# Optimization experiments

Hardware: AMD Instinct MI355X
Metric: run time of the kernel (lower is better)

Reference implementation:

```python
import jax, jax.numpy as jnp
import numpy as np

N_NODES = 500000
N_GRAPHS = 4096
D_LOCAL = 64
D_GLOBAL = 64
D_HIDDEN = 128
D_PRE = 64
LN_EPS = 1e-5


def _layer_norm(x, g, b):
    mu = jnp.mean(x, axis=-1, keepdims=True)
    var = jnp.var(x, axis=-1, keepdims=True)
    return (x - mu) * jax.lax.rsqrt(var + LN_EPS) * g + b


def setup_inputs() -> dict:
    key = jax.random.key(0)
    ks = jax.random.split(key, 16)
    s = 0.02
    d_concat = D_LOCAL + D_GLOBAL  # 128
    d_post_in = D_PRE + D_GLOBAL   # 128
    return {
        "x": jax.random.normal(ks[0], (N_NODES, D_LOCAL), jnp.float32),
        "u": jax.random.normal(ks[1], (N_GRAPHS, D_GLOBAL), jnp.float32),
        "batch": jax.random.randint(ks[2], (N_NODES,), 0, N_GRAPHS, jnp.int64),
        # mlp_pre_aggr params
        "w1": jax.random.normal(ks[3], (d_concat, D_HIDDEN), jnp.float32) * s,
        "b1": jnp.zeros((D_HIDDEN,), jnp.float32),
        "w2": jax.random.normal(ks[4], (D_HIDDEN, D_HIDDEN), jnp.float32) * s,
        "b2": jnp.zeros((D_HIDDEN,), jnp.float32),
        "w3": jax.random.normal(ks[5], (D_HIDDEN, D_PRE), jnp.float32) * s,
        "b3": jnp.zeros((D_PRE,), jnp.float32),
        "ln1_g": jnp.ones((D_PRE,), jnp.float32),
        "ln1_b": jnp.zeros((D_PRE,), jnp.float32),
        # mlp_post_aggr params
        "w4": jax.random.normal(ks[6], (d_post_in, D_HIDDEN), jnp.float32) * s,
        "b4": jnp.zeros((D_HIDDEN,), jnp.float32),
        "w5": jax.random.normal(ks[7], (D_HIDDEN, D_HIDDEN), jnp.float32) * s,
        "b5": jnp.zeros((D_HIDDEN,), jnp.float32),
        "w6": jax.random.normal(ks[8], (D_HIDDEN, D_GLOBAL), jnp.float32) * s,
        "b6": jnp.zeros((D_GLOBAL,), jnp.float32),
        "ln2_g": jnp.ones((D_GLOBAL,), jnp.float32),
        "ln2_b": jnp.zeros((D_GLOBAL,), jnp.float32),
    }


def reference(x, u, batch, w1, b1, w2, b2, w3, b3, ln1_g, ln1_b,
              w4, b4, w5, b5, w6, b6, ln2_g, ln2_b):
    # gather global state to nodes and concat: [N, dim_local + dim_global]
    h = jnp.concatenate([x, u[batch]], axis=-1)
    # mlp_pre_aggr (dropout p=0 -> identity)
    h = jax.nn.relu(h @ w1 + b1)
    h = jax.nn.relu(h @ w2 + b2)
    h = _layer_norm(h @ w3 + b3, ln1_g, ln1_b)  # [N, dim_pre_aggr]
    # scatter_add per graph
    agg = jax.ops.segment_sum(h, batch, num_segments=u.shape[0])  # [B, dim_pre_aggr]
    # concat with u, mlp_post_aggr
    g = jnp.concatenate([agg, u], axis=-1)
    g = jax.nn.relu(g @ w4 + b4)
    g = jax.nn.relu(g @ w5 + b5)
    g = _layer_norm(g @ w6 + b6, ln2_g, ln2_b)
    return g + u
```

## Files before the change

### kernel.cpp

```cpp
#include <hip/hip_runtime.h>
#include <hip/hip_bf16.h>
#include <stdint.h>


#define NNODES 500000
#define NGRAPHS 4096
#define ROWS 128
#define LDH 136

typedef __attribute__((ext_vector_type(8))) _Float16 half8;
typedef __attribute__((ext_vector_type(4))) float floatx4;

__global__ void prep_kernel(const float* __restrict__ w1, const float* __restrict__ w2,
                            const float* __restrict__ w3,
                            _Float16* __restrict__ w1T, _Float16* __restrict__ w2T,
                            _Float16* __restrict__ w3T) {
    int i = blockIdx.x * 256 + threadIdx.x;
    if (i < 128 * 128) {
        int n = i >> 7, k = i & 127;
        w1T[i] = (_Float16)w1[k * 128 + n];
        w2T[i] = (_Float16)w2[k * 128 + n];
    }
    if (i < 64 * 128) {
        int n = i >> 7, k = i & 127;
        w3T[i] = (_Float16)w3[k * 64 + n];
    }
}

__global__ __launch_bounds__(256, 2) void node_kernel(
    const float* __restrict__ x, const float* __restrict__ u, const int* __restrict__ batch,
    const _Float16* __restrict__ w1T, const _Float16* __restrict__ w2T,
    const _Float16* __restrict__ w3T,
    const float* __restrict__ b1, const float* __restrict__ b2, const float* __restrict__ b3,
    const float* __restrict__ lng, const float* __restrict__ lnb,
    float* __restrict__ agg)
{
    __shared__ __align__(16) _Float16 hA[ROWS * LDH];
    __shared__ int sBatch[ROWS];

    const int tid = threadIdx.x;
    const int rowbase = blockIdx.x * ROWS;
    const int wave = tid >> 6;
    const int lane = tid & 63;
    const int q = lane >> 4;
    const int l16 = lane & 15;

    for (int r = tid; r < ROWS; r += 256) {
        int gr = rowbase + r;
        sBatch[r] = (gr < NNODES) ? batch[gr] : 0;
    }
    __syncthreads();

    for (int i = tid; i < ROWS * 16; i += 256) {
        int r = i >> 4, c4 = (i & 15) << 2;
        int gr = rowbase + r;
        float4 vx = make_float4(0.f, 0.f, 0.f, 0.f);
        if (gr < NNODES) vx = *(const float4*)(x + (size_t)gr * 64 + c4);
        _Float16* p = &hA[r * LDH + c4];
        p[0] = (_Float16)vx.x; p[1] = (_Float16)vx.y;
        p[2] = (_Float16)vx.z; p[3] = (_Float16)vx.w;
        int g = sBatch[r];
        float4 vu = *(const float4*)(u + (size_t)g * 64 + c4);
        _Float16* p2 = &hA[r * LDH + 64 + c4];
        p2[0] = (_Float16)vu.x; p2[1] = (_Float16)vu.y;
        p2[2] = (_Float16)vu.z; p2[3] = (_Float16)vu.w;
    }
    __syncthreads();

    const int rowg = (wave >> 1) * 64;
    const int colg = (wave & 1) * 64;
    for (int layer = 0; layer < 2; ++layer) {
        const _Float16* wT = layer ? w2T : w1T;
        const float* bias = layer ? b2 : b1;
        floatx4 acc[4][4];
        #pragma unroll
        for (int ct = 0; ct < 4; ++ct) {
            float bv = bias[colg + ct * 16 + l16];
            #pragma unroll
            for (int rt = 0; rt < 4; ++rt) acc[rt][ct] = (floatx4){bv, bv, bv, bv};
        }
        half8 bfr[4][4];
        #pragma unroll
        for (int ks = 0; ks < 4; ++ks)
            #pragma unroll
            for (int ct = 0; ct < 4; ++ct)
                bfr[ks][ct] = *(const half8*)(wT + (colg + ct * 16 + l16) * 128 + ks * 32 + q * 8);
        #pragma unroll
        for (int ks = 0; ks < 4; ++ks) {
            half8 af[4];
            #pragma unroll
            for (int rt = 0; rt < 4; ++rt)
                af[rt] = *(const half8*)(&hA[(rowg + rt * 16 + l16) * LDH + ks * 32 + q * 8]);
            #pragma unroll
            for (int rt = 0; rt < 4; ++rt)
                #pragma unroll
                for (int ct = 0; ct < 4; ++ct)
                    acc[rt][ct] = __builtin_amdgcn_mfma_f32_16x16x32_f16(
                        af[rt], bfr[ks][ct], acc[rt][ct], 0, 0, 0);
        }
        __syncthreads();
        #pragma unroll
        for (int rt = 0; rt < 4; ++rt)
            #pragma unroll
            for (int ct = 0; ct < 4; ++ct)
                #pragma unroll
                for (int j = 0; j < 4; ++j) {
                    float v = acc[rt][ct][j];
                    v = v > 0.f ? v : 0.f;
                    hA[(rowg + rt * 16 + q * 4 + j) * LDH + colg + ct * 16 + l16] = (_Float16)v;
                }
        __syncthreads();
    }

    {
        const int rowg3 = wave * 32;
        floatx4 acc[2][4];
        #pragma unroll
        for (int ct = 0; ct < 4; ++ct) {
            float bv = b3[ct * 16 + l16];
            acc[0][ct] = (floatx4){bv, bv, bv, bv};
            acc[1][ct] = (floatx4){bv, bv, bv, bv};
        }
        half8 bfr[4][4];
        #pragma unroll
        for (int ks = 0; ks < 4; ++ks)
            #pragma unroll
            for (int ct = 0; ct < 4; ++ct)
                bfr[ks][ct] = *(const half8*)(w3T + (ct * 16 + l16) * 128 + ks * 32 + q * 8);
        #pragma unroll
        for (int ks = 0; ks < 4; ++ks) {
            half8 af[2];
            #pragma unroll
            for (int rt = 0; rt < 2; ++rt)
                af[rt] = *(const half8*)(&hA[(rowg3 + rt * 16 + l16) * LDH + ks * 32 + q * 8]);
            #pragma unroll
            for (int rt = 0; rt < 2; ++rt)
                #pragma unroll
                for (int ct = 0; ct < 4; ++ct)
                    acc[rt][ct] = __builtin_amdgcn_mfma_f32_16x16x32_f16(
                        af[rt], bfr[ks][ct], acc[rt][ct], 0, 0, 0);
        }
        float gct[4], bct[4];
        #pragma unroll
        for (int ct = 0; ct < 4; ++ct) {
            gct[ct] = lng[ct * 16 + l16];
            bct[ct] = lnb[ct * 16 + l16];
        }
        #pragma unroll
        for (int rt = 0; rt < 2; ++rt)
            #pragma unroll
            for (int j = 0; j < 4; ++j) {
                int rloc = rowg3 + rt * 16 + q * 4 + j;
                float v0 = acc[rt][0][j], v1 = acc[rt][1][j];
                float v2 = acc[rt][2][j], v3 = acc[rt][3][j];
                float s = v0 + v1 + v2 + v3;
                float ss = v0 * v0 + v1 * v1 + v2 * v2 + v3 * v3;
                #pragma unroll
                for (int m = 1; m < 16; m <<= 1) {
                    s += __shfl_xor(s, m, 16);
                    ss += __shfl_xor(ss, m, 16);
                }
                float mean = s * (1.f / 64.f);
                float var = ss * (1.f / 64.f) - mean * mean;
                float rstd = rsqrtf(var + 1e-5f);
                if (rowbase + rloc < NNODES) {
                    float* dst = agg + (size_t)sBatch[rloc] * 64;
                    unsafeAtomicAdd(dst + 0 + l16,  (v0 - mean) * rstd * gct[0] + bct[0]);
                    unsafeAtomicAdd(dst + 16 + l16, (v1 - mean) * rstd * gct[1] + bct[1]);
                    unsafeAtomicAdd(dst + 32 + l16, (v2 - mean) * rstd * gct[2] + bct[2]);
                    unsafeAtomicAdd(dst + 48 + l16, (v3 - mean) * rstd * gct[3] + bct[3]);
                }
            }
    }
}

__global__ __launch_bounds__(256, 4) void graph_kernel(
    const float* __restrict__ u,
    const float* __restrict__ w4, const float* __restrict__ b4,
    const float* __restrict__ w5, const float* __restrict__ b5,
    const float* __restrict__ w6, const float* __restrict__ b6,
    const float* __restrict__ g2, const float* __restrict__ bb2,
    float* __restrict__ out)
{
    __shared__ float z[4][2][128];
    const int wave = threadIdx.x >> 6, lane = threadIdx.x & 63;
    const int g = blockIdx.x * 4 + wave;
    float* za = z[wave][0];
    float* zb = z[wave][1];
    za[lane] = out[(size_t)g * 64 + lane];
    za[64 + lane] = u[(size_t)g * 64 + lane];
    float s0 = b4[lane], s1 = b4[64 + lane];
    for (int k = 0; k < 128; ++k) {
        float zk = za[k];
        s0 = fmaf(zk, w4[k * 128 + lane], s0);
        s1 = fmaf(zk, w4[k * 128 + 64 + lane], s1);
    }
    zb[lane] = fmaxf(s0, 0.f); zb[64 + lane] = fmaxf(s1, 0.f);
    s0 = b5[lane]; s1 = b5[64 + lane];
    for (int k = 0; k < 128; ++k) {
        float zk = zb[k];
        s0 = fmaf(zk, w5[k * 128 + lane], s0);
        s1 = fmaf(zk, w5[k * 128 + 64 + lane], s1);
    }
    za[lane] = fmaxf(s0, 0.f); za[64 + lane] = fmaxf(s1, 0.f);
    float s = b6[lane];
    for (int k = 0; k < 128; ++k) s = fmaf(za[k], w6[k * 64 + lane], s);
    float sum = s, ssq = s * s;
    #pragma unroll
    for (int m = 1; m < 64; m <<= 1) {
        sum += __shfl_xor(sum, m, 64);
        ssq += __shfl_xor(ssq, m, 64);
    }
    float mean = sum * (1.f / 64.f);
    float var = ssq * (1.f / 64.f) - mean * mean;
    float rstd = rsqrtf(var + 1e-5f);
    out[(size_t)g * 64 + lane] =
        (s - mean) * rstd * g2[lane] + bb2[lane] + u[(size_t)g * 64 + lane];
}

extern "C" void kernel_launch(void* const* d_in, const int* in_sizes, int n_in,
                              void* d_out, int out_size, void* d_ws, size_t ws_size,
                              hipStream_t stream) {
    const float* x   = (const float*)d_in[0];
    const float* u   = (const float*)d_in[1];
    const int*   bt  = (const int*)d_in[2];
    const float* w1  = (const float*)d_in[3];
    const float* b1  = (const float*)d_in[4];
    const float* w2  = (const float*)d_in[5];
    const float* b2  = (const float*)d_in[6];
    const float* w3  = (const float*)d_in[7];
    const float* b3  = (const float*)d_in[8];
    const float* lng = (const float*)d_in[9];
    const float* lnb = (const float*)d_in[10];
    const float* w4  = (const float*)d_in[11];
    const float* b4  = (const float*)d_in[12];
    const float* w5  = (const float*)d_in[13];
    const float* b5  = (const float*)d_in[14];
    const float* w6  = (const float*)d_in[15];
    const float* b6  = (const float*)d_in[16];
    const float* g2  = (const float*)d_in[17];
    const float* bb2 = (const float*)d_in[18];
    float* out = (float*)d_out;

    _Float16* w1T = (_Float16*)d_ws;
    _Float16* w2T = w1T + 128 * 128;
    _Float16* w3T = w2T + 128 * 128;

    hipMemsetAsync(d_out, 0, (size_t)NGRAPHS * 64 * sizeof(float), stream);
    prep_kernel<<<64, 256, 0, stream>>>(w1, w2, w3, w1T, w2T, w3T);
    node_kernel<<<(NNODES + ROWS - 1) / ROWS, 256, 0, stream>>>(
        x, u, bt, w1T, w2T, w3T, b1, b2, b3, lng, lnb, out);
    graph_kernel<<<NGRAPHS / 4, 256, 0, stream>>>(
        u, w4, b4, w5, b5, w6, b6, g2, bb2, out);
}
```

Before: 408.4 us.

## Sort nodes by graph and fuse per-graph node MLP, aggregation and post-MLP

Builds a counting sort of nodes by graph id (histogram, scan, scatter) and launches one block per graph. Each block gathers its nodes' x rows, runs the three-layer node MLP and layer norm, sums the results in registers and runs the post-aggregation MLP directly. This removes the float atomics into agg and the separate graph kernel. The u part of the first layer is computed once per graph as a bias, halving that layer's K dimension. The cost is three extra small kernels, gathered x loads, and uneven per-graph work with only 4096 blocks and partially filled last tiles.

Result: slower. 707.7 us (+73.3%).

```diff
diff --git a/kernel.cpp b/kernel.cpp
--- a/kernel.cpp
+++ b/kernel.cpp
@@ -5,7 +5,6 @@
 
 #define NNODES 500000
 #define NGRAPHS 4096
-#define ROWS 128
 #define LDH 136
 
 typedef __attribute__((ext_vector_type(8))) _Float16 half8;
@@ -27,195 +26,303 @@
     }
 }
 
-__global__ __launch_bounds__(256, 2) void node_kernel(
-    const float* __restrict__ x, const float* __restrict__ u, const int* __restrict__ batch,
+__global__ void hist_kernel(const int* __restrict__ batch, int* __restrict__ cnt) {
+    int i = blockIdx.x * 256 + threadIdx.x;
+    if (i < NNODES) atomicAdd(&cnt[batch[i]], 1);
+}
+
+__global__ void scan_kernel(const int* __restrict__ cnt, int* __restrict__ offs) {
+    __shared__ int ssum[256];
+    int t = threadIdx.x;
+    int base = t * 16;
+    int s = 0;
+    #pragma unroll
+    for (int j = 0; j < 16; ++j) s += cnt[base + j];
+    ssum[t] = s;
+    __syncthreads();
+    for (int d = 1; d < 256; d <<= 1) {
+        int v = (t >= d) ? ssum[t - d] : 0;
+        __syncthreads();
+        ssum[t] += v;
+        __syncthreads();
+    }
+    int run = ssum[t] - s;
+    #pragma unroll
+    for (int j = 0; j < 16; ++j) { offs[base + j] = run; run += cnt[base + j]; }
+    if (t == 255) offs[4096] = run;
+}
+
+__global__ void scatter_kernel(const int* __restrict__ batch, const int* __restrict__ offs,
+                               int* __restrict__ cursor, int* __restrict__ sorted) {
+    int i = blockIdx.x * 256 + threadIdx.x;
+    if (i < NNODES) {
+        int g = batch[i];
+        int p = offs[g] + atomicAdd(&cursor[g], 1);
+        sorted[p] = i;
+    }
+}
+
+__global__ __launch_bounds__(256, 4) void node_fused(
+    const float* __restrict__ x, const float* __restrict__ u,
+    const int* __restrict__ sorted, const int* __restrict__ offs,
     const _Float16* __restrict__ w1T, const _Float16* __restrict__ w2T,
     const _Float16* __restrict__ w3T,
     const float* __restrict__ b1, const float* __restrict__ b2, const float* __restrict__ b3,
     const float* __restrict__ lng, const float* __restrict__ lnb,
-    float* __restrict__ agg)
-{
-    __shared__ __align__(16) _Float16 hA[ROWS * LDH];
-    __shared__ int sBatch[ROWS];
-
-    const int tid = threadIdx.x;
-    const int rowbase = blockIdx.x * ROWS;
-    const int wave = tid >> 6;
-    const int lane = tid & 63;
-    const int q = lane >> 4;
-    const int l16 = lane & 15;
-
-    for (int r = tid; r < ROWS; r += 256) {
-        int gr = rowbase + r;
-        sBatch[r] = (gr < NNODES) ? batch[gr] : 0;
-    }
-    __syncthreads();
-
-    for (int i = tid; i < ROWS * 16; i += 256) {
-        int r = i >> 4, c4 = (i & 15) << 2;
-        int gr = rowbase + r;
-        float4 vx = make_float4(0.f, 0.f, 0.f, 0.f);
-        if (gr < NNODES) vx = *(const float4*)(x + (size_t)gr * 64 + c4);
-        _Float16* p = &hA[r * LDH + c4];
-        p[0] = (_Float16)vx.x; p[1] = (_Float16)vx.y;
-        p[2] = (_Float16)vx.z; p[3] = (_Float16)vx.w;
-        int g = sBatch[r];
-        float4 vu = *(const float4*)(u + (size_t)g * 64 + c4);
-        _Float16* p2 = &hA[r * LDH + 64 + c4];
-        p2[0] = (_Float16)vu.x; p2[1] = (_Float16)vu.y;
-        p2[2] = (_Float16)vu.z; p2[3] = (_Float16)vu.w;
-    }
-    __syncthreads();
-
-    const int rowg = (wave >> 1) * 64;
-    const int colg = (wave & 1) * 64;
-    for (int layer = 0; layer < 2; ++layer) {
-        const _Float16* wT = layer ? w2T : w1T;
-        const float* bias = layer ? b2 : b1;
-        floatx4 acc[4][4];
-        #pragma unroll
-        for (int ct = 0; ct < 4; ++ct) {
-            float bv = bias[colg + ct * 16 + l16];
-            #pragma unroll
-            for (int rt = 0; rt < 4; ++rt) acc[rt][ct] = (floatx4){bv, bv, bv, bv};
-        }
-        half8 bfr[4][4];
-        #pragma unroll
-        for (int ks = 0; ks < 4; ++ks)
-            #pragma unroll
-            for (int ct = 0; ct < 4; ++ct)
-                bfr[ks][ct] = *(const half8*)(wT + (colg + ct * 16 + l16) * 128 + ks * 32 + q * 8);
-        #pragma unroll
-        for (int ks = 0; ks < 4; ++ks) {
-            half8 af[4];
-            #pragma unroll
-            for (int rt = 0; rt < 4; ++rt)
-                af[rt] = *(const half8*)(&hA[(rowg + rt * 16 + l16) * LDH + ks * 32 + q * 8]);
-            #pragma unroll
-            for (int rt = 0; rt < 4; ++rt)
-                #pragma unroll
-                for (int ct = 0; ct < 4; ++ct)
-                    acc[rt][ct] = __builtin_amdgcn_mfma_f32_16x16x32_f16(
-                        af[rt], bfr[ks][ct], acc[rt][ct], 0, 0, 0);
-        }
-        __syncthreads();
-        #pragma unroll
-        for (int rt = 0; rt < 4; ++rt)
-            #pragma unroll
-            for (int ct = 0; ct < 4; ++ct)
-                #pragma unroll
-                for (int j = 0; j < 4; ++j) {
-                    float v = acc[rt][ct][j];
-                    v = v > 0.f ? v : 0.f;
-                    hA[(rowg + rt * 16 + q * 4 + j) * LDH + colg + ct * 16 + l16] = (_Float16)v;
-                }
-        __syncthreads();
-    }
-
-    {
-        const int rowg3 = wave * 32;
-        floatx4 acc[2][4];
-        #pragma unroll
-        for (int ct = 0; ct < 4; ++ct) {
-            float bv = b3[ct * 16 + l16];
-            acc[0][ct] = (floatx4){bv, bv, bv, bv};
-            acc[1][ct] = (floatx4){bv, bv, bv, bv};
-        }
-        half8 bfr[4][4];
-        #pragma unroll
-        for (int ks = 0; ks < 4; ++ks)
-            #pragma unroll
-            for (int ct = 0; ct < 4; ++ct)
-                bfr[ks][ct] = *(const half8*)(w3T + (ct * 16 + l16) * 128 + ks * 32 + q * 8);
-        #pragma unroll
-        for (int ks = 0; ks < 4; ++ks) {
-            half8 af[2];
-            #pragma unroll
-            for (int rt = 0; rt < 2; ++rt)
-                af[rt] = *(const half8*)(&hA[(rowg3 + rt * 16 + l16) * LDH + ks * 32 + q * 8]);
-            #pragma unroll
-            for (int rt = 0; rt < 2; ++rt)
-                #pragma unroll
-                for (int ct = 0; ct < 4; ++ct)
-                    acc[rt][ct] = __builtin_amdgcn_mfma_f32_16x16x32_f16(
-                        af[rt], bfr[ks][ct], acc[rt][ct], 0, 0, 0);
-        }
-        float gct[4], bct[4];
-        #pragma unroll
-        for (int ct = 0; ct < 4; ++ct) {
-            gct[ct] = lng[ct * 16 + l16];
-            bct[ct] = lnb[ct * 16 + l16];
-        }
-        #pragma unroll
-        for (int rt = 0; rt < 2; ++rt)
-            #pragma unroll
-            for (int j = 0; j < 4; ++j) {
-                int rloc = rowg3 + rt * 16 + q * 4 + j;
-                float v0 = acc[rt][0][j], v1 = acc[rt][1][j];
-                float v2 = acc[rt][2][j], v3 = acc[rt][3][j];
-                float s = v0 + v1 + v2 + v3;
-                float ss = v0 * v0 + v1 * v1 + v2 * v2 + v3 * v3;
-                #pragma unroll
-                for (int m = 1; m < 16; m <<= 1) {
-                    s += __shfl_xor(s, m, 16);
-                    ss += __shfl_xor(ss, m, 16);
-                }
-                float mean = s * (1.f / 64.f);
-                float var = ss * (1.f / 64.f) - mean * mean;
-                float rstd = rsqrtf(var + 1e-5f);
-                if (rowbase + rloc < NNODES) {
-                    float* dst = agg + (size_t)sBatch[rloc] * 64;
-                    unsafeAtomicAdd(dst + 0 + l16,  (v0 - mean) * rstd * gct[0] + bct[0]);
-                    unsafeAtomicAdd(dst + 16 + l16, (v1 - mean) * rstd * gct[1] + bct[1]);
-                    unsafeAtomicAdd(dst + 32 + l16, (v2 - mean) * rstd * gct[2] + bct[2]);
-                    unsafeAtomicAdd(dst + 48 + l16, (v3 - mean) * rstd * gct[3] + bct[3]);
-                }
-            }
-    }
-}
-
-__global__ __launch_bounds__(256, 4) void graph_kernel(
-    const float* __restrict__ u,
     const float* __restrict__ w4, const float* __restrict__ b4,
     const float* __restrict__ w5, const float* __restrict__ b5,
     const float* __restrict__ w6, const float* __restrict__ b6,
     const float* __restrict__ g2, const float* __restrict__ bb2,
     float* __restrict__ out)
 {
-    __shared__ float z[4][2][128];
-    const int wave = threadIdx.x >> 6, lane = threadIdx.x & 63;
-    const int g = blockIdx.x * 4 + wave;
-    float* za = z[wave][0];
-    float* zb = z[wave][1];
-    za[lane] = out[(size_t)g * 64 + lane];
-    za[64 + lane] = u[(size_t)g * 64 + lane];
-    float s0 = b4[lane], s1 = b4[64 + lane];
-    for (int k = 0; k < 128; ++k) {
-        float zk = za[k];
-        s0 = fmaf(zk, w4[k * 128 + lane], s0);
-        s1 = fmaf(zk, w4[k * 128 + 64 + lane], s1);
-    }
-    zb[lane] = fmaxf(s0, 0.f); zb[64 + lane] = fmaxf(s1, 0.f);
-    s0 = b5[lane]; s1 = b5[64 + lane];
-    for (int k = 0; k < 128; ++k) {
-        float zk = zb[k];
-        s0 = fmaf(zk, w5[k * 128 + lane], s0);
-        s1 = fmaf(zk, w5[k * 128 + 64 + lane], s1);
-    }
-    za[lane] = fmaxf(s0, 0.f); za[64 + lane] = fmaxf(s1, 0.f);
-    float s = b6[lane];
-    for (int k = 0; k < 128; ++k) s = fmaf(za[k], w6[k * 64 + lane], s);
-    float sum = s, ssq = s * s;
+    __shared__ __align__(16) _Float16 hA[128 * LDH];
+    __shared__ int sIdx[128];
+    __shared__ float uf[64];
+    __shared__ float ub[128];
+    __shared__ float waveacc[4][64];
+    __shared__ float zf[128], h1[128], pbuf[2][128];
+
+    const int g = blockIdx.x;
+    const int tid = threadIdx.x;
+    const int wave = tid >> 6;
+    const int lane = tid & 63;
+    const int q = lane >> 4;
+    const int l16 = lane & 15;
+    const int beg = offs[g];
+    const int cnt = offs[g + 1] - beg;
+
+    if (tid < 64) uf[tid] = u[(size_t)g * 64 + tid];
+    __syncthreads();
+    if (tid < 128) {
+        float s = b1[tid];
+        const _Float16* wp = w1T + tid * 128 + 64;
+        #pragma unroll
+        for (int k = 0; k < 64; ++k) s += uf[k] * (float)wp[k];
+        ub[tid] = s;
+    }
+
+    float regacc[4] = {0.f, 0.f, 0.f, 0.f};
+    const int ntiles = (cnt + 127) >> 7;
+    const int rowg = (wave >> 1) * 64;
+    const int colg = (wave & 1) * 64;
+    const int rowg3 = wave * 32;
+
+    for (int t = 0; t < ntiles; ++t) {
+        if (tid < 128) {
+            int rr = t * 128 + tid;
+            sIdx[tid] = (rr < cnt) ? sorted[beg + rr] : -1;
+        }
+        __syncthreads();
+        for (int i = tid; i < 128 * 16; i += 256) {
+            int r = i >> 4, c4 = (i & 15) << 2;
+            int idx = sIdx[r];
+            float4 v = make_float4(0.f, 0.f, 0.f, 0.f);
+            if (idx >= 0) v = *(const float4*)(x + (size_t)idx * 64 + c4);
+            _Float16* p = &hA[r * LDH + c4];
+            p[0] = (_Float16)v.x; p[1] = (_Float16)v.y;
+            p[2] = (_Float16)v.z; p[3] = (_Float16)v.w;
+        }
+        __syncthreads();
+
+        {
+            floatx4 acc[4][4];
+            #pragma unroll
+            for (int ct = 0; ct < 4; ++ct) {
+                float bv = ub[colg + ct * 16 + l16];
+                #pragma unroll
+                for (int rt = 0; rt < 4; ++rt) acc[rt][ct] = (floatx4){bv, bv, bv, bv};
+            }
+            half8 bfr[2][4];
+            #pragma unroll
+            for (int ks = 0; ks < 2; ++ks)
+                #pragma unroll
+                for (int ct = 0; ct < 4; ++ct)
+                    bfr[ks][ct] = *(const half8*)(w1T + (colg + ct * 16 + l16) * 128 + ks * 32 + q * 8);
+            #pragma unroll
+            for (int ks = 0; ks < 2; ++ks) {
+                half8 af[4];
+                #pragma unroll
+                for (int rt = 0; rt < 4; ++rt)
+                    af[rt] = *(const half8*)(&hA[(rowg + rt * 16 + l16) * LDH + ks * 32 + q * 8]);
+                #pragma unroll
+                for (int rt = 0; rt < 4; ++rt)
+                    #pragma unroll
+                    for (int ct = 0; ct < 4; ++ct)
+                        acc[rt][ct] = __builtin_amdgcn_mfma_f32_16x16x32_f16(
+                            af[rt], bfr[ks][ct], acc[rt][ct], 0, 0, 0);
+            }
+            __syncthreads();
+            #pragma unroll
+            for (int rt = 0; rt < 4; ++rt)
+                #pragma unroll
+                for (int ct = 0; ct < 4; ++ct)
+                    #pragma unroll
+                    for (int j = 0; j < 4; ++j) {
+                        float v = acc[rt][ct][j];
+                        v = v > 0.f ? v : 0.f;
+                        hA[(rowg + rt * 16 + q * 4 + j) * LDH + colg + ct * 16 + l16] = (_Float16)v;
+                    }
+            __syncthreads();
+        }
+
+        {
+            floatx4 acc[4][4];
+            #pragma unroll
+            for (int ct = 0; ct < 4; ++ct) {
+                float bv = b2[colg + ct * 16 + l16];
+                #pragma unroll
+                for (int rt = 0; rt < 4; ++rt) acc[rt][ct] = (floatx4){bv, bv, bv, bv};
+            }
+            half8 bfr[4][4];
+            #pragma unroll
+            for (int ks = 0; ks < 4; ++ks)
+                #pragma unroll
+                for (int ct = 0; ct < 4; ++ct)
+                    bfr[ks][ct] = *(const half8*)(w2T + (colg + ct * 16 + l16) * 128 + ks * 32 + q * 8);
+            #pragma unroll
+            for (int ks = 0; ks < 4; ++ks) {
+                half8 af[4];
+                #pragma unroll
+                for (int rt = 0; rt < 4; ++rt)
+                    af[rt] = *(const half8*)(&hA[(rowg + rt * 16 + l16) * LDH + ks * 32 + q * 8]);
+                #pragma unroll
+                for (int rt = 0; rt < 4; ++rt)
+                    #pragma unroll
+                    for (int ct = 0; ct < 4; ++ct)
+                        acc[rt][ct] = __builtin_amdgcn_mfma_f32_16x16x32_f16(
+                            af[rt], bfr[ks][ct], acc[rt][ct], 0, 0, 0);
+            }
+            __syncthreads();
+            #pragma unroll
+            for (int rt = 0; rt < 4; ++rt)
+                #pragma unroll
+                for (int ct = 0; ct < 4; ++ct)
+                    #pragma unroll
+                    for (int j = 0; j < 4; ++j) {
+                        float v = acc[rt][ct][j];
+                        v = v > 0.f ? v : 0.f;
+                        hA[(rowg + rt * 16 + q * 4 + j) * LDH + colg + ct * 16 + l16] = (_Float16)v;
+                    }
+            __syncthreads();
+        }
+
+        {
+            floatx4 acc[2][4];
+            #pragma unroll
+            for (int ct = 0; ct < 4; ++ct) {
+                float bv = b3[ct * 16 + l16];
+                acc[0][ct] = (floatx4){bv, bv, bv, bv};
+                acc[1][ct] = (floatx4){bv, bv, bv, bv};
+            }
+            half8 bfr[4][4];
+            #pragma unroll
+            for (int ks = 0; ks < 4; ++ks)
+                #pragma unroll
+                for (int ct = 0; ct < 4; ++ct)
+                    bfr[ks][ct] = *(const half8*)(w3T + (ct * 16 + l16) * 128 + ks * 32 + q * 8);
+            #pragma unroll
+            for (int ks = 0; ks < 4; ++ks) {
+                half8 af[2];
+                #pragma unroll
+                for (int rt = 0; rt < 2; ++rt)
+                    af[rt] = *(const half8*)(&hA[(rowg3 + rt * 16 + l16) * LDH + ks * 32 + q * 8]);
+                #pragma unroll
+                for (int rt = 0; rt < 2; ++rt)
+                    #pragma unroll
+                    for (int ct = 0; ct < 4; ++ct)
+                        acc[rt][ct] = __builtin_amdgcn_mfma_f32_16x16x32_f16(
+                            af[rt], bfr[ks][ct], acc[rt][ct], 0, 0, 0);
+            }
+            float gct[4], bct[4];
+            #pragma unroll
+            for (int ct = 0; ct < 4; ++ct) {
+                gct[ct] = lng[ct * 16 + l16];
+                bct[ct] = lnb[ct * 16 + l16];
+            }
+            #pragma unroll
+            for (int rt = 0; rt < 2; ++rt)
+                #pragma unroll
+                for (int j = 0; j < 4; ++j) {
+                    int rloc = rowg3 + rt * 16 + q * 4 + j;
+                    float v0 = acc[rt][0][j], v1 = acc[rt][1][j];
+                    float v2 = acc[rt][2][j], v3 = acc[rt][3][j];
+                    float s = v0 + v1 + v2 + v3;
+                    float ss = v0 * v0 + v1 * v1 + v2 * v2 + v3 * v3;
+                    #pragma unroll
+                    for (int m = 1; m < 16; m <<= 1) {
+                        s += __shfl_xor(s, m, 16);
+                        ss += __shfl_xor(ss, m, 16);
+                    }
+                    float mean = s * (1.f / 64.f);
+                    float var = ss * (1.f / 64.f) - mean * mean;
+                    float rstd = rsqrtf(var + 1e-5f);
+                    if (t * 128 + rloc < cnt) {
+                        regacc[0] += (v0 - mean) * rstd * gct[0] + bct[0];
+                        regacc[1] += (v1 - mean) * rstd * gct[1] + bct[1];
+                        regacc[2] += (v2 - mean) * rstd * gct[2] + bct[2];
+                        regacc[3] += (v3 - mean) * rstd * gct[3] + bct[3];
+                    }
+                }
+            __syncthreads();
+        }
+    }
+
     #pragma unroll
-    for (int m = 1; m < 64; m <<= 1) {
-        sum += __shfl_xor(sum, m, 64);
-        ssq += __shfl_xor(ssq, m, 64);
-    }
-    float mean = sum * (1.f / 64.f);
-    float var = ssq * (1.f / 64.f) - mean * mean;
-    float rstd = rsqrtf(var + 1e-5f);
-    out[(size_t)g * 64 + lane] =
-        (s - mean) * rstd * g2[lane] + bb2[lane] + u[(size_t)g * 64 + lane];
+    for (int ct = 0; ct < 4; ++ct) {
+        float v = regacc[ct];
+        v += __shfl_xor(v, 16, 64);
+        v += __shfl_xor(v, 32, 64);
+        if (lane < 16) waveacc[wave][ct * 16 + lane] = v;
+    }
+    __syncthreads();
+    if (tid < 64) {
+        float a = waveacc[0][tid] + waveacc[1][tid] + waveacc[2][tid] + waveacc[3][tid];
+        zf[tid] = a;
+        zf[64 + tid] = uf[tid];
+    }
+    __syncthreads();
+
+    {
+        int n = tid & 127, half = tid >> 7;
+        float s = half ? 0.f : b4[n];
+        #pragma unroll 16
+        for (int k = 0; k < 64; ++k) s = fmaf(zf[half * 64 + k], w4[(half * 64 + k) * 128 + n], s);
+        pbuf[half][n] = s;
+    }
+    __syncthreads();
+    if (tid < 128) h1[tid] = fmaxf(pbuf[0][tid] + pbuf[1][tid], 0.f);
+    __syncthreads();
+    {
+        int n = tid & 127, half = tid >> 7;
+        float s = half ? 0.f : b5[n];
+        #pragma unroll 16
+        for (int k = 0; k < 64; ++k) s = fmaf(h1[half * 64 + k], w5[(half * 64 + k) * 128 + n], s);
+        pbuf[half][n] = s;
+    }
+    __syncthreads();
+    if (tid < 128) zf[tid] = fmaxf(pbuf[0][tid] + pbuf[1][tid], 0.f);
+    __syncthreads();
+    if (tid < 128) {
+        int n = tid & 63, half = (tid >> 6) & 1;
+        float s = half ? 0.f : b6[n];
+        #pragma unroll 16
+        for (int k = 0; k < 64; ++k) s = fmaf(zf[half * 64 + k], w6[(half * 64 + k) * 64 + n], s);
+        pbuf[half][n] = s;
+    }
+    __syncthreads();
+    if (tid < 64) {
+        float s = pbuf[0][tid] + pbuf[1][tid];
+        float sum = s, ssq = s * s;
+        #pragma unroll
+        for (int m = 1; m < 64; m <<= 1) {
+            sum += __shfl_xor(sum, m, 64);
+            ssq += __shfl_xor(ssq, m, 64);
+        }
+        float mean = sum * (1.f / 64.f);
+        float var = ssq * (1.f / 64.f) - mean * mean;
+        float rstd = rsqrtf(var + 1e-5f);
+        out[(size_t)g * 64 + tid] = (s - mean) * rstd * g2[tid] + bb2[tid] + uf[tid];
+    }
 }
 
 extern "C" void kernel_launch(void* const* d_in, const int* in_sizes, int n_in,
@@ -242,14 +349,21 @@
     const float* bb2 = (const float*)d_in[18];
     float* out = (float*)d_out;
 
-    _Float16* w1T = (_Float16*)d_ws;
-    _Float16* w2T = w1T + 128 * 128;
-    _Float16* w3T = w2T + 128 * 128;
-
-    hipMemsetAsync(d_out, 0, (size_t)NGRAPHS * 64 * sizeof(float), stream);
+    char* p = (char*)d_ws;
+    _Float16* w1T   = (_Float16*)p;            p += 128 * 128 * 2;
+    _Float16* w2T   = (_Float16*)p;            p += 128 * 128 * 2;
+    _Float16* w3T   = (_Float16*)p;            p += 64 * 128 * 2;
+    int* cnt        = (int*)p;                 p += 4096 * 4;
+    int* cursor     = (int*)p;                 p += 4096 * 4;
+    int* offs       = (int*)p;                 p += 4100 * 4;
+    int* sorted     = (int*)p;                 p += NNODES * 4;
+
+    hipMemsetAsync(cnt, 0, 2 * 4096 * sizeof(int), stream);
     prep_kernel<<<64, 256, 0, stream>>>(w1, w2, w3, w1T, w2T, w3T);
-    node_kernel<<<(NNODES + ROWS - 1) / ROWS, 256, 0, stream>>>(
-        x, u, bt, w1T, w2T, w3T, b1, b2, b3, lng, lnb, out);
-    graph_kernel<<<NGRAPHS / 4, 256, 0, stream>>>(
-        u, w4, b4, w5, b5, w6, b6, g2, bb2, out);
-}
+    hist_kernel<<<(NNODES + 255) / 256, 256, 0, stream>>>(bt, cnt);
+    scan_kernel<<<1, 256, 0, stream>>>(cnt, offs);
+    scatter_kernel<<<(NNODES + 255) / 256, 256, 0, stream>>>(bt, offs, cursor, sorted);
+    node_fused<<<NGRAPHS, 256, 0, stream>>>(
+        x, u, sorted, offs, w1T, w2T, w3T, b1, b2, b3, lng, lnb,
+        w4, b4, w5, b5, w6, b6, g2, bb2, out);
+}
```
